# Performance work log

Hardware: AMD Instinct MI355X
Metric: run time of the kernel (lower is better)

## Reference

```python
import jax, jax.numpy as jnp
import numpy as np

TAU = 0.1
EPS = 1e-20


def _gumbel_softmax_hard(logits, gumbels, tau):
    # logits: [4], gumbels: [B, S, 4]
    y_soft = jax.nn.softmax((logits + gumbels) / tau, axis=-1)
    y_hard = jax.nn.one_hot(jnp.argmax(y_soft, axis=-1), logits.shape[-1], dtype=y_soft.dtype)
    # straight-through estimator (matches F.gumbel_softmax(hard=True))
    return y_hard + y_soft - jax.lax.stop_gradient(y_soft)


def _forward(mean, outcomeA, outcomeB, BEVa, BEVb, kapa):
    B, _, S = outcomeA.shape
    g_key = jax.random.key(42)
    u = jax.random.uniform(g_key, (B, S, 4), dtype=mean.dtype)
    gumbels = -jnp.log(-jnp.log(u + EPS) + EPS)  # standard Gumbel(0,1) noise
    logits = jax.nn.log_softmax(mean)            # F.log_softmax(m)
    p = _gumbel_softmax_hard(logits, gumbels, TAU)          # [B, S, 4] one-hot (ST)
    mask = (jnp.arange(S)[None, :] < kapa[:, None]).astype(p.dtype)  # s < kapa[b]
    denom = kapa.astype(p.dtype)
    # STa[b] = (1/kapa[b]) * sum_{s<kapa[b]} outcomeA[b,:,s] @ p[b,s]
    sta = jnp.einsum('bks,bsk,bs->b', outcomeA, p, mask) / denom
    stb = jnp.einsum('bks,bsk,bs->b', outcomeB, p, mask) / denom
    return jax.nn.sigmoid(BEVb - BEVa + stb - sta)  # [B]


def setup_inputs() -> dict:
    key = jax.random.key(0)
    B, S = 16384, 256
    k = jax.random.split(key, 6)
    return {
        'outcomeA': jax.random.normal(k[0], (B, 4, S), dtype=jnp.float32),
        'outcomeB': jax.random.normal(k[1], (B, 4, S), dtype=jnp.float32),
        'BEVa': jax.random.normal(k[2], (B,), dtype=jnp.float32),
        'BEVb': jax.random.normal(k[3], (B,), dtype=jnp.float32),
        'kapa': jax.random.randint(k[4], (B,), 1, S + 1, dtype=jnp.int32),
        'batch_size': B,
        'features': jax.random.normal(k[5], (B, 35), dtype=jnp.float32),
        'mean': jnp.array([2.0, 1.0, 1.0, 1.0], dtype=jnp.float32),
    }


def reference(outcomeA, outcomeB, BEVa, BEVb, kapa, batch_size, features, mean):
    # features is dead code in the original forward (MLP commented out)
    del batch_size, features
    return _forward(mean, outcomeA, outcomeB, BEVa, BEVb, kapa)
```

## Files before the change

kernel.cpp:

```cpp
#include <hip/hip_runtime.h>
#include <stdint.h>
#include <math.h>


__device__ __forceinline__ uint32_t rotl32(uint32_t x, int r) {
    return (x << r) | (x >> (32 - r));
}

__device__ __forceinline__ uint32_t tf2x32_xor(uint32_t c0, uint32_t c1) {
    const uint32_t ks0 = 0u, ks1 = 42u, ks2 = 0x1BD11BF0u;
    uint32_t x0 = c0 + ks0, x1 = c1 + ks1;
#define TF_R(r) { x0 += x1; x1 = rotl32(x1, r); x1 ^= x0; }
    TF_R(13) TF_R(15) TF_R(26) TF_R(6)
    x0 += ks1; x1 += ks2 + 1u;
    TF_R(17) TF_R(29) TF_R(16) TF_R(24)
    x0 += ks2; x1 += ks0 + 2u;
    TF_R(13) TF_R(15) TF_R(26) TF_R(6)
    x0 += ks0; x1 += ks1 + 3u;
    TF_R(17) TF_R(29) TF_R(16) TF_R(24)
    x0 += ks1; x1 += ks2 + 4u;
    TF_R(13) TF_R(15) TF_R(26) TF_R(6)
    x0 += ks2; x1 += ks0 + 5u;
#undef TF_R
    return x0 ^ x1;
}

__device__ __forceinline__ float fast_w(uint32_t m ) {
    const float u = (float)m * 0x1p-23f;
    if (u > 0.96875f) {
        const float d  = (float)(0x800000u - m) * 0x1p-23f;
        const float d2 = d * d;
        return d + d2 * (0.5f + d * (0.333333333f + d * (0.25f + d * 0.2f)));
    }
    return -__logf(u + 1e-20f);
}

__global__ __launch_bounds__(256) void bayes_kernel(
    const float* __restrict__ A,
    const float* __restrict__ Bo,
    const float* __restrict__ BEVa,
    const float* __restrict__ BEVb,
    const int*   __restrict__ kapa,
    const float* __restrict__ mean,
    float*       __restrict__ out)
{
    const int b = blockIdx.x;
    const int s = threadIdx.x;
    const int kp = kapa[b];

    int ksel = 0;
    if (s < kp) {
        const float m0 = mean[0], m1 = mean[1], m2 = mean[2], m3 = mean[3];
        const float mx = fmaxf(fmaxf(m0, m1), fmaxf(m2, m3));
        const float c[4] = { m0 - mx, m1 - mx, m2 - mx, m3 - mx };

        const uint32_t i0 = ((uint32_t)(b * 256 + s)) * 4u;
        uint32_t bits[4];
        float sc[4];
#pragma unroll
        for (int k = 0; k < 4; ++k) {
            bits[k] = tf2x32_xor(0u, i0 + (uint32_t)k);
            sc[k]   = c[k] - __logf(fast_w(bits[k] >> 9));
        }

        float b1 = sc[0], b2 = -3.4e38f;
        ksel = 0;
#pragma unroll
        for (int k = 1; k < 4; ++k) {
            if (sc[k] > b1)      { b2 = b1; b1 = sc[k]; ksel = k; }
            else if (sc[k] > b2) { b2 = sc[k]; }
        }

        if (b1 - b2 < 5e-4f) {
            double best = -1.0e308;
            ksel = 0;
#pragma unroll
            for (int k = 0; k < 4; ++k) {
                const double u = (double)((float)(bits[k] >> 9) * 0x1p-23f);
                const double w = -log(u + 1e-20) + 1e-20;
                const double sk = ((double)c[k]) - log(w);
                if (sk > best) { best = sk; ksel = k; }
            }
        }
    }

    float av = 0.0f, bv = 0.0f;
    if (s < kp) {
        const int off = (b * 4 + ksel) * 256 + s;
        av = A[off];
        bv = Bo[off];
    }

#pragma unroll
    for (int off = 32; off >= 1; off >>= 1) {
        av += __shfl_down(av, off);
        bv += __shfl_down(bv, off);
    }

    __shared__ float red[4][2];
    const int wid  = threadIdx.x >> 6;
    const int lane = threadIdx.x & 63;
    if (lane == 0) { red[wid][0] = av; red[wid][1] = bv; }
    __syncthreads();

    if (threadIdx.x == 0) {
        float sA = 0.f, sB = 0.f;
#pragma unroll
        for (int w = 0; w < 4; ++w) { sA += red[w][0]; sB += red[w][1]; }
        const double d = (double)kp;
        const double x = (double)BEVb[b] - (double)BEVa[b]
                       + (double)sB / d - (double)sA / d;
        out[b] = (float)(1.0 / (1.0 + exp(-x)));
    }
}

extern "C" void kernel_launch(void* const* d_in, const int* in_sizes, int n_in,
                              void* d_out, int out_size, void* d_ws, size_t ws_size,
                              hipStream_t stream) {
    (void)in_sizes; (void)n_in; (void)d_ws; (void)ws_size; (void)out_size;
    const float* A    = (const float*)d_in[0];
    const float* Bo   = (const float*)d_in[1];
    const float* BEVa = (const float*)d_in[2];
    const float* BEVb = (const float*)d_in[3];
    const int*   kapa = (const int*)d_in[4];
    const float* mean = (const float*)d_in[7];
    float* out = (float*)d_out;

    bayes_kernel<<<16384, 256, 0, stream>>>(A, Bo, BEVa, BEVb, kapa, mean, out);
}
```

Before: 164.2 us.

## Map one wavefront per batch row and add grouped-logit argmax shortcut

Each 64-lane wavefront now handles one batch row, looping over four sequence chunks. This removes the shared-memory reduction and __syncthreads, and the grid shrinks from 16384 to 4096 blocks. When the last three mean entries are equal, the argmax among those three is taken on the raw integer bits, so only two log evaluations are needed instead of four. The fast_w branch is made branchless, at the cost of always evaluating both paths, and per-row loads become serial within a wave, which may reduce memory-level parallelism.

Measured after the change: 158.7 us. 3.3% less time.

```diff
diff --git a/kernel.cpp b/kernel.cpp
--- a/kernel.cpp
+++ b/kernel.cpp
@@ -26,13 +26,18 @@
 }
 
 __device__ __forceinline__ float fast_w(uint32_t m ) {
-    const float u = (float)m * 0x1p-23f;
-    if (u > 0.96875f) {
-        const float d  = (float)(0x800000u - m) * 0x1p-23f;
-        const float d2 = d * d;
-        return d + d2 * (0.5f + d * (0.333333333f + d * (0.25f + d * 0.2f)));
-    }
-    return -__logf(u + 1e-20f);
+    const float u  = (float)m * 0x1p-23f;
+    const float wl = -__logf(u + 1e-20f);
+    const float d  = (float)(0x800000u - m) * 0x1p-23f;
+    const float d2 = d * d;
+    const float ws = d + d2 * (0.5f + d * (0.333333333f + d * (0.25f + d * 0.2f)));
+    return (u > 0.96875f) ? ws : wl;
+}
+
+__device__ __forceinline__ double exact_lw(uint32_t m) {
+    const double u = (double)m * 0x1p-23;
+    const double w = -log(u + 1e-20) + 1e-20;
+    return log(w);
 }
 
 __global__ __launch_bounds__(256) void bayes_kernel(
@@ -44,51 +49,68 @@
     const float* __restrict__ mean,
     float*       __restrict__ out)
 {
-    const int b = blockIdx.x;
-    const int s = threadIdx.x;
-    const int kp = kapa[b];
+    const int wid  = threadIdx.x >> 6;
+    const int lane = threadIdx.x & 63;
+    const int b    = (blockIdx.x << 2) | wid;
+    const int kp   = kapa[b];
 
-    int ksel = 0;
-    if (s < kp) {
-        const float m0 = mean[0], m1 = mean[1], m2 = mean[2], m3 = mean[3];
-        const float mx = fmaxf(fmaxf(m0, m1), fmaxf(m2, m3));
-        const float c[4] = { m0 - mx, m1 - mx, m2 - mx, m3 - mx };
+    const float m0 = mean[0], m1 = mean[1], m2 = mean[2], m3 = mean[3];
+    const float mx = fmaxf(fmaxf(m0, m1), fmaxf(m2, m3));
+    const float c0 = m0 - mx, c1 = m1 - mx, c2 = m2 - mx, c3 = m3 - mx;
+    const bool grouped = (c1 == c2) && (c2 == c3);
 
-        const uint32_t i0 = ((uint32_t)(b * 256 + s)) * 4u;
-        uint32_t bits[4];
-        float sc[4];
-#pragma unroll
-        for (int k = 0; k < 4; ++k) {
-            bits[k] = tf2x32_xor(0u, i0 + (uint32_t)k);
-            sc[k]   = c[k] - __logf(fast_w(bits[k] >> 9));
-        }
-
-        float b1 = sc[0], b2 = -3.4e38f;
-        ksel = 0;
-#pragma unroll
-        for (int k = 1; k < 4; ++k) {
-            if (sc[k] > b1)      { b2 = b1; b1 = sc[k]; ksel = k; }
-            else if (sc[k] > b2) { b2 = sc[k]; }
-        }
-
-        if (b1 - b2 < 5e-4f) {
-            double best = -1.0e308;
-            ksel = 0;
-#pragma unroll
-            for (int k = 0; k < 4; ++k) {
-                const double u = (double)((float)(bits[k] >> 9) * 0x1p-23f);
-                const double w = -log(u + 1e-20) + 1e-20;
-                const double sk = ((double)c[k]) - log(w);
-                if (sk > best) { best = sk; ksel = k; }
-            }
-        }
-    }
+    const float* __restrict__ Arow = A  + (size_t)b * 1024;
+    const float* __restrict__ Brow = Bo + (size_t)b * 1024;
 
     float av = 0.0f, bv = 0.0f;
-    if (s < kp) {
-        const int off = (b * 4 + ksel) * 256 + s;
-        av = A[off];
-        bv = Bo[off];
+#pragma unroll
+    for (int j = 0; j < 4; ++j) {
+        const int s = lane + (j << 6);
+        if (s < kp) {
+            const uint32_t i0 = ((uint32_t)(b * 256 + s)) << 2;
+            uint32_t m[4];
+#pragma unroll
+            for (int k = 0; k < 4; ++k)
+                m[k] = tf2x32_xor(0u, i0 + (uint32_t)k) >> 9;
+
+            int ksel;
+            if (grouped) {
+                int jg = 1; uint32_t mm = m[1];
+                if (m[2] > mm) { mm = m[2]; jg = 2; }
+                if (m[3] > mm) { mm = m[3]; jg = 3; }
+                const float s0f = c0 - __logf(fast_w(m[0]));
+                const float sjf = c1 - __logf(fast_w(mm));
+                ksel = (s0f >= sjf) ? 0 : jg;
+                if (fabsf(s0f - sjf) < 5e-4f) {
+                    const double S0 = (double)c0 - exact_lw(m[0]);
+                    const double Sj = (double)c1 - exact_lw(mm);
+                    ksel = (S0 >= Sj) ? 0 : jg;
+                }
+            } else {
+                const float cc[4] = { c0, c1, c2, c3 };
+                float sc[4];
+#pragma unroll
+                for (int k = 0; k < 4; ++k)
+                    sc[k] = cc[k] - __logf(fast_w(m[k]));
+                float b1 = sc[0], b2 = -3.4e38f; ksel = 0;
+#pragma unroll
+                for (int k = 1; k < 4; ++k) {
+                    if (sc[k] > b1)      { b2 = b1; b1 = sc[k]; ksel = k; }
+                    else if (sc[k] > b2) { b2 = sc[k]; }
+                }
+                if (b1 - b2 < 5e-4f) {
+                    double best = -1.0e308; ksel = 0;
+#pragma unroll
+                    for (int k = 0; k < 4; ++k) {
+                        const double sk = (double)cc[k] - exact_lw(m[k]);
+                        if (sk > best) { best = sk; ksel = k; }
+                    }
+                }
+            }
+            const int off = (ksel << 8) + s;
+            av += Arow[off];
+            bv += Brow[off];
+        }
     }
 
 #pragma unroll
@@ -97,19 +119,10 @@
         bv += __shfl_down(bv, off);
     }
 
-    __shared__ float red[4][2];
-    const int wid  = threadIdx.x >> 6;
-    const int lane = threadIdx.x & 63;
-    if (lane == 0) { red[wid][0] = av; red[wid][1] = bv; }
-    __syncthreads();
-
-    if (threadIdx.x == 0) {
-        float sA = 0.f, sB = 0.f;
-#pragma unroll
-        for (int w = 0; w < 4; ++w) { sA += red[w][0]; sB += red[w][1]; }
+    if (lane == 0) {
         const double d = (double)kp;
         const double x = (double)BEVb[b] - (double)BEVa[b]
-                       + (double)sB / d - (double)sA / d;
+                       + (double)bv / d - (double)av / d;
         out[b] = (float)(1.0 / (1.0 + exp(-x)));
     }
 }
@@ -126,5 +139,5 @@
     const float* mean = (const float*)d_in[7];
     float* out = (float*)d_out;
 
-    bayes_kernel<<<16384, 256, 0, stream>>>(A, Bo, BEVa, BEVb, kapa, mean, out);
+    bayes_kernel<<<4096, 256, 0, stream>>>(A, Bo, BEVa, BEVb, kapa, mean, out);
 }
```
